# Optimization experiments

Measured on AMD Instinct MI355X. Metric: run time of the kernel, lower is better.

## Reference

```python
import jax, jax.numpy as jnp
import numpy as np

WH, WW = 8, 8
N_TOK = WH * WW
NUM_HEADS = 4
DIM = 128
B_WIN = 4096  # num_windows * B
NW = 64       # windows per image (for mask)


def _make_rel_tables():
    # relative coords table (1, 2*Wh-1, 2*Ww-1, 2), log-spaced as in SwinV2
    ch = np.arange(-(WH - 1), WH, dtype=np.float32)
    cw = np.arange(-(WW - 1), WW, dtype=np.float32)
    t = np.stack(np.meshgrid(ch, cw, indexing='ij'), axis=-1)[None]  # (1,15,15,2)
    t[..., 0] /= (WH - 1)
    t[..., 1] /= (WW - 1)
    t *= 8
    t = np.sign(t) * np.log2(np.abs(t) + 1.0) / np.log2(8)
    # relative position index (N, N)
    coords = np.stack(np.meshgrid(np.arange(WH), np.arange(WW), indexing='ij'))
    cf = coords.reshape(2, -1)
    rel = cf[:, :, None] - cf[:, None, :]
    rel = rel.transpose(1, 2, 0).copy()
    rel[:, :, 0] += WH - 1
    rel[:, :, 1] += WW - 1
    rel[:, :, 0] *= 2 * WW - 1
    idx = rel.sum(-1).astype(np.int32)
    return jnp.asarray(t), jnp.asarray(idx)


def setup_inputs() -> dict:
    key = jax.random.key(0)
    ks = jax.random.split(key, 8)
    table, idx = _make_rel_tables()
    return {
        'x': jax.random.normal(ks[0], (B_WIN, N_TOK, DIM), jnp.float32),
        'context': jax.random.normal(ks[1], (B_WIN, N_TOK, DIM), jnp.float32),
        'mask': jnp.zeros((NW, N_TOK, N_TOK), jnp.float32),
        'q_w': jax.random.normal(ks[2], (DIM, DIM), jnp.float32) * 0.02,
        'q_b': jnp.zeros((DIM,), jnp.float32),
        'kv_w': jax.random.normal(ks[3], (2 * DIM, DIM), jnp.float32) * 0.02,
        'v_b': jnp.zeros((DIM,), jnp.float32),
        'logit_scale': jnp.full((NUM_HEADS, 1, 1), np.log(10.0), jnp.float32),
        'cpb_w1': jax.random.normal(ks[4], (512, 2), jnp.float32) * 0.02,
        'cpb_b1': jnp.zeros((512,), jnp.float32),
        'cpb_w2': jax.random.normal(ks[5], (NUM_HEADS, 512), jnp.float32) * 0.02,
        'proj_w': jax.random.normal(ks[6], (DIM, DIM), jnp.float32) * 0.02,
        'proj_b': jnp.zeros((DIM,), jnp.float32),
        'rel_coords_table': table,
        'rel_pos_index': idx,
    }


def _l2norm(t, eps=1e-12):
    return t / jnp.maximum(jnp.linalg.norm(t, axis=-1, keepdims=True), eps)


def reference(x, context, mask, q_w, q_b, kv_w, v_b, logit_scale,
              cpb_w1, cpb_b1, cpb_w2, proj_w, proj_b,
              rel_coords_table, rel_pos_index):
    B_, N, C = x.shape
    H = NUM_HEADS
    hd = C // H
    # projections (kv bias = [zeros_like(v_b); v_b])
    q = x @ q_w.T + q_b
    kv_bias = jnp.concatenate([jnp.zeros_like(v_b), v_b])
    kv = context @ kv_w.T + kv_bias
    q = q.reshape(B_, N, H, hd).transpose(0, 2, 1, 3)          # (B_,H,N,hd)
    kv = kv.reshape(B_, N, 2, H, hd).transpose(2, 0, 3, 1, 4)  # (2,B_,H,N,hd)
    k, v = kv[0], kv[1]
    # cosine attention with clamped learned scale
    attn = jnp.einsum('bhnd,bhmd->bhnm', _l2norm(q), _l2norm(k))
    scale = jnp.exp(jnp.minimum(logit_scale, np.log(1.0 / 0.01)))  # (H,1,1)
    attn = attn * scale[None]
    # CPB-MLP relative position bias
    hidd = jax.nn.relu(rel_coords_table @ cpb_w1.T + cpb_b1)   # (1,15,15,512)
    table = (hidd @ cpb_w2.T).reshape(-1, H)                   # ((2Wh-1)(2Ww-1), H)
    bias = table[rel_pos_index.reshape(-1)].reshape(N, N, H)
    bias = 16.0 * jax.nn.sigmoid(bias.transpose(2, 0, 1))      # (H,N,N)
    attn = attn + bias[None]
    # shift mask
    nW = mask.shape[0]
    attn = attn.reshape(B_ // nW, nW, H, N, N) + mask[None, :, None]
    attn = attn.reshape(B_, H, N, N)
    attn = jax.nn.softmax(attn, axis=-1)
    out = jnp.einsum('bhnm,bhmd->bhnd', attn, v)
    out = out.transpose(0, 2, 1, 3).reshape(B_, N, C)
    return out @ proj_w.T + proj_b
```

## Files before the change

kernel.cpp:

```cpp
#include <hip/hip_runtime.h>
#include <hip/hip_bf16.h>

#define NT 64
#define DIM 128
#define NH 4
#define HD 32

typedef __attribute__((ext_vector_type(8))) short short8;
typedef __attribute__((ext_vector_type(4))) short short4v;
typedef __attribute__((ext_vector_type(8))) __bf16 bf16x8;
typedef __attribute__((ext_vector_type(4))) float floatx4;

__device__ __forceinline__ short f2bf(float f) {
  unsigned u = __builtin_bit_cast(unsigned, f);
  u += 0x7FFFu + ((u >> 16) & 1u);
  return (short)(u >> 16);
}

__device__ __forceinline__ bf16x8 ldsfrag(const short* p) {
  return __builtin_bit_cast(bf16x8, *(const short8*)p);
}

__device__ __forceinline__ bf16x8 wfrag(const float* p) {
  float4 a = *(const float4*)p;
  float4 b = *(const float4*)(p + 4);
  short8 v;
  v[0]=f2bf(a.x); v[1]=f2bf(a.y); v[2]=f2bf(a.z); v[3]=f2bf(a.w);
  v[4]=f2bf(b.x); v[5]=f2bf(b.y); v[6]=f2bf(b.z); v[7]=f2bf(b.w);
  return __builtin_bit_cast(bf16x8, v);
}

#define MFMA(a,b,c) __builtin_amdgcn_mfma_f32_16x16x32_bf16(a,b,c,0,0,0)

__device__ __forceinline__ void stage_tile(const float* __restrict__ src, short* dst_base, int tid) {
  int r = tid >> 2, c0 = (tid & 3) * 32;
  const float4* s = (const float4*)(src + r * DIM + c0);
  short* dst = dst_base + r * 136 + c0;
#pragma unroll
  for (int i = 0; i < 4; ++i) {
    float4 a = s[2*i], b = s[2*i+1];
    short8 v;
    v[0]=f2bf(a.x); v[1]=f2bf(a.y); v[2]=f2bf(a.z); v[3]=f2bf(a.w);
    v[4]=f2bf(b.x); v[5]=f2bf(b.y); v[6]=f2bf(b.z); v[7]=f2bf(b.w);
    *(short8*)(dst + i*8) = v;
  }
}

__global__ void cpb_bias_kernel(const float* __restrict__ table,
                                const float* __restrict__ w1,
                                const float* __restrict__ b1,
                                const float* __restrict__ w2,
                                const int*   __restrict__ idx,
                                float* __restrict__ bias_packed) {
  __shared__ float logits[225][4];
  int t = threadIdx.x;
  if (t < 225) {
    float t0 = table[2*t], t1 = table[2*t+1];
    float a0=0.f, a1=0.f, a2=0.f, a3=0.f;
    for (int j = 0; j < 512; ++j) {
      float h = fmaxf(0.f, t0 * w1[2*j] + t1 * w1[2*j+1] + b1[j]);
      a0 += h * w2[j];
      a1 += h * w2[512 + j];
      a2 += h * w2[1024 + j];
      a3 += h * w2[1536 + j];
    }
    logits[t][0]=a0; logits[t][1]=a1; logits[t][2]=a2; logits[t][3]=a3;
  }
  __syncthreads();
  for (int f = t; f < 16384; f += 256) {
    int i    = f & 3;
    int lane = (f >> 2) & 63;
    int nt   = (f >> 8) & 3;
    int mt   = (f >> 10) & 3;
    int h    = (f >> 12) & 3;
    int r = mt*16 + (lane >> 4)*4 + i;
    int c = nt*16 + (lane & 15);
    int p = idx[r*64 + c];
    float v = logits[p][h];
    bias_packed[f] = 16.f / (1.f + __expf(-v));
  }
}

__global__ __launch_bounds__(256, 2)
void swin_ctx_attn_kernel(const float* __restrict__ x, const float* __restrict__ ctx,
                          const float* __restrict__ mask,
                          const float* __restrict__ q_w, const float* __restrict__ q_b,
                          const float* __restrict__ kv_w, const float* __restrict__ v_b,
                          const float* __restrict__ logit_scale,
                          const float* __restrict__ proj_w, const float* __restrict__ proj_b,
                          const float* __restrict__ bias_p,
                          float* __restrict__ out) {
  __shared__ short lds[38400] __attribute__((aligned(16)));
  const int tid  = threadIdx.x;
  const int lane = tid & 63;
  const int w    = tid >> 6;
  const int b    = blockIdx.x;
  const int lr   = lane & 15;
  const int lg   = lane >> 4;

  short* stage = lds;
  short* hb    = lds + 8704 + w * 7424;
  short* qn    = hb;
  short* kn    = hb + 2560;
  short* attnb = hb;
  short* vT    = hb + 5120;

  stage_tile(x + (size_t)b * (NT*DIM), stage, tid);
  __syncthreads();

  {
    floatx4 acc[4][2] = {};
    for (int ks = 0; ks < 4; ++ks) {
      bf16x8 A[4];
#pragma unroll
      for (int mt = 0; mt < 4; ++mt)
        A[mt] = ldsfrag(stage + (mt*16 + lr)*136 + ks*32 + lg*8);
#pragma unroll
      for (int nt = 0; nt < 2; ++nt) {
        bf16x8 B = wfrag(q_w + (size_t)(w*32 + nt*16 + lr)*DIM + ks*32 + lg*8);
#pragma unroll
        for (int mt = 0; mt < 4; ++mt)
          acc[mt][nt] = MFMA(A[mt], B, acc[mt][nt]);
      }
    }
    float qb0 = q_b[w*32 + lr], qb1 = q_b[w*32 + 16 + lr];
#pragma unroll
    for (int mt = 0; mt < 4; ++mt) {
      floatx4 ss;
#pragma unroll
      for (int i = 0; i < 4; ++i) {
        acc[mt][0][i] += qb0; acc[mt][1][i] += qb1;
        ss[i] = acc[mt][0][i]*acc[mt][0][i] + acc[mt][1][i]*acc[mt][1][i];
      }
      for (int m = 1; m < 16; m <<= 1)
#pragma unroll
        for (int i = 0; i < 4; ++i) ss[i] += __shfl_xor(ss[i], m, 64);
#pragma unroll
      for (int i = 0; i < 4; ++i) {
        float sc = 1.0f / fmaxf(sqrtf(ss[i]), 1e-12f);
        int row = mt*16 + lg*4 + i;
        qn[row*40 + lr]      = f2bf(acc[mt][0][i] * sc);
        qn[row*40 + 16 + lr] = f2bf(acc[mt][1][i] * sc);
      }
    }
  }
  __syncthreads();

  stage_tile(ctx + (size_t)b * (NT*DIM), stage, tid);
  __syncthreads();

  {
    floatx4 acc[4][2] = {};
    for (int ks = 0; ks < 4; ++ks) {
      bf16x8 A[4];
#pragma unroll
      for (int mt = 0; mt < 4; ++mt)
        A[mt] = ldsfrag(stage + (mt*16 + lr)*136 + ks*32 + lg*8);
#pragma unroll
      for (int nt = 0; nt < 2; ++nt) {
        bf16x8 B = wfrag(kv_w + (size_t)(w*32 + nt*16 + lr)*DIM + ks*32 + lg*8);
#pragma unroll
        for (int mt = 0; mt < 4; ++mt)
          acc[mt][nt] = MFMA(A[mt], B, acc[mt][nt]);
      }
    }
#pragma unroll
    for (int mt = 0; mt < 4; ++mt) {
      floatx4 ss;
#pragma unroll
      for (int i = 0; i < 4; ++i)
        ss[i] = acc[mt][0][i]*acc[mt][0][i] + acc[mt][1][i]*acc[mt][1][i];
      for (int m = 1; m < 16; m <<= 1)
#pragma unroll
        for (int i = 0; i < 4; ++i) ss[i] += __shfl_xor(ss[i], m, 64);
#pragma unroll
      for (int i = 0; i < 4; ++i) {
        float sc = 1.0f / fmaxf(sqrtf(ss[i]), 1e-12f);
        int row = mt*16 + lg*4 + i;
        kn[row*40 + lr]      = f2bf(acc[mt][0][i] * sc);
        kn[row*40 + 16 + lr] = f2bf(acc[mt][1][i] * sc);
      }
    }
  }

  {
    floatx4 acc[4][2] = {};
    for (int ks = 0; ks < 4; ++ks) {
      bf16x8 A[4];
#pragma unroll
      for (int mt = 0; mt < 4; ++mt)
        A[mt] = ldsfrag(stage + (mt*16 + lr)*136 + ks*32 + lg*8);
#pragma unroll
      for (int nt = 0; nt < 2; ++nt) {
        bf16x8 B = wfrag(kv_w + (size_t)(DIM + w*32 + nt*16 + lr)*DIM + ks*32 + lg*8);
#pragma unroll
        for (int mt = 0; mt < 4; ++mt)
          acc[mt][nt] = MFMA(A[mt], B, acc[mt][nt]);
      }
    }
    float vb0 = v_b[w*32 + lr], vb1 = v_b[w*32 + 16 + lr];
#pragma unroll
    for (int mt = 0; mt < 4; ++mt)
#pragma unroll
      for (int nt = 0; nt < 2; ++nt) {
        float vb = nt ? vb1 : vb0;
        short4v s4;
#pragma unroll
        for (int i = 0; i < 4; ++i) s4[i] = f2bf(acc[mt][nt][i] + vb);
        *(short4v*)(vT + (nt*16 + lr)*72 + mt*16 + lg*4) = s4;
      }
  }
  asm volatile("s_waitcnt lgkmcnt(0)" ::: "memory");

  floatx4 sacc[4][4] = {};
  {
    bf16x8 A[4];
#pragma unroll
    for (int mt = 0; mt < 4; ++mt)
      A[mt] = ldsfrag(qn + (mt*16 + lr)*40 + lg*8);
#pragma unroll
    for (int nt = 0; nt < 4; ++nt) {
      bf16x8 B = ldsfrag(kn + (nt*16 + lr)*40 + lg*8);
#pragma unroll
      for (int mt = 0; mt < 4; ++mt)
        sacc[mt][nt] = MFMA(A[mt], B, sacc[mt][nt]);
    }
  }

  {
    float scl = expf(fminf(logit_scale[w], 4.605170185988091f));
    int wimg = b & 63;
#pragma unroll
    for (int mt = 0; mt < 4; ++mt)
#pragma unroll
      for (int nt = 0; nt < 4; ++nt) {
        floatx4 bias4 = ((const floatx4*)bias_p)[(w*16 + mt*4 + nt)*64 + lane];
#pragma unroll
        for (int i = 0; i < 4; ++i) {
          int r = mt*16 + lg*4 + i, c = nt*16 + lr;
          sacc[mt][nt][i] = sacc[mt][nt][i]*scl + bias4[i] + mask[((size_t)wimg*64 + r)*64 + c];
        }
      }
#pragma unroll
    for (int mt = 0; mt < 4; ++mt) {
      floatx4 rmax;
#pragma unroll
      for (int i = 0; i < 4; ++i)
        rmax[i] = fmaxf(fmaxf(sacc[mt][0][i], sacc[mt][1][i]), fmaxf(sacc[mt][2][i], sacc[mt][3][i]));
      for (int m = 1; m < 16; m <<= 1)
#pragma unroll
        for (int i = 0; i < 4; ++i) rmax[i] = fmaxf(rmax[i], __shfl_xor(rmax[i], m, 64));
      floatx4 rsum = {};
#pragma unroll
      for (int nt = 0; nt < 4; ++nt)
#pragma unroll
        for (int i = 0; i < 4; ++i) {
          sacc[mt][nt][i] = __expf(sacc[mt][nt][i] - rmax[i]);
          rsum[i] += sacc[mt][nt][i];
        }
      for (int m = 1; m < 16; m <<= 1)
#pragma unroll
        for (int i = 0; i < 4; ++i) rsum[i] += __shfl_xor(rsum[i], m, 64);
#pragma unroll
      for (int i = 0; i < 4; ++i) rsum[i] = 1.0f / rsum[i];
#pragma unroll
      for (int nt = 0; nt < 4; ++nt)
#pragma unroll
        for (int i = 0; i < 4; ++i) sacc[mt][nt][i] *= rsum[i];
    }
  }

#pragma unroll
  for (int mt = 0; mt < 4; ++mt)
#pragma unroll
    for (int nt = 0; nt < 4; ++nt)
#pragma unroll
      for (int i = 0; i < 4; ++i)
        attnb[(mt*16 + lg*4 + i)*72 + nt*16 + lr] = f2bf(sacc[mt][nt][i]);
  asm volatile("s_waitcnt lgkmcnt(0)" ::: "memory");

  floatx4 oacc[4][2] = {};
  for (int ks = 0; ks < 2; ++ks) {
    bf16x8 A[4];
#pragma unroll
    for (int mt = 0; mt < 4; ++mt)
      A[mt] = ldsfrag(attnb + (mt*16 + lr)*72 + ks*32 + lg*8);
#pragma unroll
    for (int nt = 0; nt < 2; ++nt) {
      bf16x8 B = ldsfrag(vT + (nt*16 + lr)*72 + ks*32 + lg*8);
#pragma unroll
      for (int mt = 0; mt < 4; ++mt)
        oacc[mt][nt] = MFMA(A[mt], B, oacc[mt][nt]);
    }
  }

  __syncthreads();
#pragma unroll
  for (int mt = 0; mt < 4; ++mt)
#pragma unroll
    for (int nt = 0; nt < 2; ++nt)
#pragma unroll
      for (int i = 0; i < 4; ++i)
        stage[(mt*16 + lg*4 + i)*136 + w*32 + nt*16 + lr] = f2bf(oacc[mt][nt][i]);
  __syncthreads();

  {
    floatx4 acc[4][2] = {};
    for (int ks = 0; ks < 4; ++ks) {
      bf16x8 A[4];
#pragma unroll
      for (int mt = 0; mt < 4; ++mt)
        A[mt] = ldsfrag(stage + (mt*16 + lr)*136 + ks*32 + lg*8);
#pragma unroll
      for (int nt = 0; nt < 2; ++nt) {
        bf16x8 B = wfrag(proj_w + (size_t)(w*32 + nt*16 + lr)*DIM + ks*32 + lg*8);
#pragma unroll
        for (int mt = 0; mt < 4; ++mt)
          acc[mt][nt] = MFMA(A[mt], B, acc[mt][nt]);
      }
    }
    float pb0 = proj_b[w*32 + lr], pb1 = proj_b[w*32 + 16 + lr];
    float* outp = out + (size_t)b * (NT*DIM);
#pragma unroll
    for (int mt = 0; mt < 4; ++mt)
#pragma unroll
      for (int nt = 0; nt < 2; ++nt) {
        float pb = nt ? pb1 : pb0;
#pragma unroll
        for (int i = 0; i < 4; ++i)
          outp[(mt*16 + lg*4 + i)*DIM + w*32 + nt*16 + lr] = acc[mt][nt][i] + pb;
      }
  }
}

extern "C" void kernel_launch(void* const* d_in, const int* in_sizes, int n_in,
                              void* d_out, int out_size, void* d_ws, size_t ws_size,
                              hipStream_t stream) {
  const float* x     = (const float*)d_in[0];
  const float* ctx   = (const float*)d_in[1];
  const float* mask  = (const float*)d_in[2];
  const float* q_w   = (const float*)d_in[3];
  const float* q_b   = (const float*)d_in[4];
  const float* kv_w  = (const float*)d_in[5];
  const float* v_b   = (const float*)d_in[6];
  const float* ls    = (const float*)d_in[7];
  const float* w1    = (const float*)d_in[8];
  const float* b1    = (const float*)d_in[9];
  const float* w2    = (const float*)d_in[10];
  const float* pw    = (const float*)d_in[11];
  const float* pb    = (const float*)d_in[12];
  const float* table = (const float*)d_in[13];
  const int*   idx   = (const int*)d_in[14];

  float* bias_p = (float*)d_ws;
  int B = in_sizes[0] / (NT * DIM);

  cpb_bias_kernel<<<1, 256, 0, stream>>>(table, w1, b1, w2, idx, bias_p);
  swin_ctx_attn_kernel<<<B, 256, 0, stream>>>(x, ctx, mask, q_w, q_b, kv_w, v_b,
                                              ls, pw, pb, bias_p, (float*)d_out);
}
```

Before: 321.8 us.

## Pre-convert weights to bf16 and split each head across two waves with 512 threads

```diff
diff --git a/kernel.cpp b/kernel.cpp
--- a/kernel.cpp
+++ b/kernel.cpp
@@ -21,314 +21,343 @@
   return __builtin_bit_cast(bf16x8, *(const short8*)p);
 }
 
-__device__ __forceinline__ bf16x8 wfrag(const float* p) {
-  float4 a = *(const float4*)p;
-  float4 b = *(const float4*)(p + 4);
-  short8 v;
-  v[0]=f2bf(a.x); v[1]=f2bf(a.y); v[2]=f2bf(a.z); v[3]=f2bf(a.w);
-  v[4]=f2bf(b.x); v[5]=f2bf(b.y); v[6]=f2bf(b.z); v[7]=f2bf(b.w);
-  return __builtin_bit_cast(bf16x8, v);
-}
-
 #define MFMA(a,b,c) __builtin_amdgcn_mfma_f32_16x16x32_bf16(a,b,c,0,0,0)
 
-__device__ __forceinline__ void stage_tile(const float* __restrict__ src, short* dst_base, int tid) {
-  int r = tid >> 2, c0 = (tid & 3) * 32;
-  const float4* s = (const float4*)(src + r * DIM + c0);
-  short* dst = dst_base + r * 136 + c0;
-#pragma unroll
-  for (int i = 0; i < 4; ++i) {
-    float4 a = s[2*i], b = s[2*i+1];
-    short8 v;
-    v[0]=f2bf(a.x); v[1]=f2bf(a.y); v[2]=f2bf(a.z); v[3]=f2bf(a.w);
-    v[4]=f2bf(b.x); v[5]=f2bf(b.y); v[6]=f2bf(b.z); v[7]=f2bf(b.w);
-    *(short8*)(dst + i*8) = v;
-  }
-}
-
-__global__ void cpb_bias_kernel(const float* __restrict__ table,
-                                const float* __restrict__ w1,
-                                const float* __restrict__ b1,
-                                const float* __restrict__ w2,
-                                const int*   __restrict__ idx,
-                                float* __restrict__ bias_packed) {
-  __shared__ float logits[225][4];
+__global__ void prep_kernel(const float* __restrict__ table,
+                            const float* __restrict__ w1,
+                            const float* __restrict__ b1,
+                            const float* __restrict__ w2,
+                            const int*   __restrict__ idx,
+                            const float* __restrict__ q_w,
+                            const float* __restrict__ kv_w,
+                            const float* __restrict__ proj_w,
+                            float* __restrict__ bias_packed,
+                            short* __restrict__ wbf) {
   int t = threadIdx.x;
-  if (t < 225) {
-    float t0 = table[2*t], t1 = table[2*t+1];
-    float a0=0.f, a1=0.f, a2=0.f, a3=0.f;
-    for (int j = 0; j < 512; ++j) {
-      float h = fmaxf(0.f, t0 * w1[2*j] + t1 * w1[2*j+1] + b1[j]);
-      a0 += h * w2[j];
-      a1 += h * w2[512 + j];
-      a2 += h * w2[1024 + j];
-      a3 += h * w2[1536 + j];
-    }
-    logits[t][0]=a0; logits[t][1]=a1; logits[t][2]=a2; logits[t][3]=a3;
-  }
-  __syncthreads();
-  for (int f = t; f < 16384; f += 256) {
-    int i    = f & 3;
-    int lane = (f >> 2) & 63;
-    int nt   = (f >> 8) & 3;
-    int mt   = (f >> 10) & 3;
-    int h    = (f >> 12) & 3;
-    int r = mt*16 + (lane >> 4)*4 + i;
-    int c = nt*16 + (lane & 15);
-    int p = idx[r*64 + c];
-    float v = logits[p][h];
-    bias_packed[f] = 16.f / (1.f + __expf(-v));
-  }
-}
-
-__global__ __launch_bounds__(256, 2)
+  if (blockIdx.x == 0) {
+    __shared__ float logits[225][4];
+    if (t < 225) {
+      float t0 = table[2*t], t1 = table[2*t+1];
+      float a0=0.f, a1=0.f, a2=0.f, a3=0.f;
+      for (int j = 0; j < 512; ++j) {
+        float h = fmaxf(0.f, t0 * w1[2*j] + t1 * w1[2*j+1] + b1[j]);
+        a0 += h * w2[j];
+        a1 += h * w2[512 + j];
+        a2 += h * w2[1024 + j];
+        a3 += h * w2[1536 + j];
+      }
+      logits[t][0]=a0; logits[t][1]=a1; logits[t][2]=a2; logits[t][3]=a3;
+    }
+    __syncthreads();
+    for (int f = t; f < 16384; f += 256) {
+      int i    = f & 3;
+      int lane = (f >> 2) & 63;
+      int nt   = (f >> 8) & 3;
+      int mt   = (f >> 10) & 3;
+      int h    = (f >> 12) & 3;
+      int r = mt*16 + (lane >> 4)*4 + i;
+      int c = nt*16 + (lane & 15);
+      int p = idx[r*64 + c];
+      float v = logits[p][h];
+      bias_packed[f] = 16.f / (1.f + __expf(-v));
+    }
+  } else {
+    int gidx = (blockIdx.x - 1) * 4096 + t * 16;
+    const float* src; int off;
+    if (gidx < 16384)      { src = q_w;    off = gidx; }
+    else if (gidx < 49152) { src = kv_w;   off = gidx - 16384; }
+    else                   { src = proj_w; off = gidx - 49152; }
+    const float4* s = (const float4*)(src + off);
+    short* dst = wbf + gidx;
+#pragma unroll
+    for (int i = 0; i < 2; ++i) {
+      float4 a = s[2*i], b = s[2*i+1];
+      short8 v;
+      v[0]=f2bf(a.x); v[1]=f2bf(a.y); v[2]=f2bf(a.z); v[3]=f2bf(a.w);
+      v[4]=f2bf(b.x); v[5]=f2bf(b.y); v[6]=f2bf(b.z); v[7]=f2bf(b.w);
+      *(short8*)(dst + i*8) = v;
+    }
+  }
+}
+
+__global__ __launch_bounds__(512, 4)
 void swin_ctx_attn_kernel(const float* __restrict__ x, const float* __restrict__ ctx,
                           const float* __restrict__ mask,
-                          const float* __restrict__ q_w, const float* __restrict__ q_b,
-                          const float* __restrict__ kv_w, const float* __restrict__ v_b,
+                          const short* __restrict__ wq, const float* __restrict__ q_b,
+                          const short* __restrict__ wkv, const float* __restrict__ v_b,
                           const float* __restrict__ logit_scale,
-                          const float* __restrict__ proj_w, const float* __restrict__ proj_b,
+                          const short* __restrict__ wproj, const float* __restrict__ proj_b,
                           const float* __restrict__ bias_p,
                           float* __restrict__ out) {
   __shared__ short lds[38400] __attribute__((aligned(16)));
   const int tid  = threadIdx.x;
   const int lane = tid & 63;
-  const int w    = tid >> 6;
+  const int wv   = tid >> 6;
+  const int h    = wv >> 1;
+  const int s    = wv & 1;
   const int b    = blockIdx.x;
   const int lr   = lane & 15;
   const int lg   = lane >> 4;
 
   short* stage = lds;
-  short* hb    = lds + 8704 + w * 7424;
+  short* hb    = lds + 8704 + h * 7424;
   short* qn    = hb;
   short* kn    = hb + 2560;
   short* attnb = hb;
   short* vT    = hb + 5120;
 
-  stage_tile(x + (size_t)b * (NT*DIM), stage, tid);
-  __syncthreads();
-
-  {
-    floatx4 acc[4][2] = {};
+  const int sr = tid >> 3, sc = (tid & 7) * 16;
+  {
+    const float4* sx = (const float4*)(x + (size_t)b * (NT*DIM) + sr*DIM + sc);
+    short* d = stage + sr*136 + sc;
+#pragma unroll
+    for (int i = 0; i < 2; ++i) {
+      float4 a = sx[2*i], bb = sx[2*i+1];
+      short8 v;
+      v[0]=f2bf(a.x); v[1]=f2bf(a.y); v[2]=f2bf(a.z); v[3]=f2bf(a.w);
+      v[4]=f2bf(bb.x); v[5]=f2bf(bb.y); v[6]=f2bf(bb.z); v[7]=f2bf(bb.w);
+      *(short8*)(d + i*8) = v;
+    }
+  }
+  float4 cr[4];
+  {
+    const float4* cs = (const float4*)(ctx + (size_t)b * (NT*DIM) + sr*DIM + sc);
+#pragma unroll
+    for (int i = 0; i < 4; ++i) cr[i] = cs[i];
+  }
+  __syncthreads();
+
+  {
+    floatx4 acc[2][2] = {};
     for (int ks = 0; ks < 4; ++ks) {
-      bf16x8 A[4];
-#pragma unroll
-      for (int mt = 0; mt < 4; ++mt)
-        A[mt] = ldsfrag(stage + (mt*16 + lr)*136 + ks*32 + lg*8);
-#pragma unroll
-      for (int nt = 0; nt < 2; ++nt) {
-        bf16x8 B = wfrag(q_w + (size_t)(w*32 + nt*16 + lr)*DIM + ks*32 + lg*8);
-#pragma unroll
-        for (int mt = 0; mt < 4; ++mt)
-          acc[mt][nt] = MFMA(A[mt], B, acc[mt][nt]);
-      }
-    }
-    float qb0 = q_b[w*32 + lr], qb1 = q_b[w*32 + 16 + lr];
-#pragma unroll
-    for (int mt = 0; mt < 4; ++mt) {
+      bf16x8 A[2];
+#pragma unroll
+      for (int m = 0; m < 2; ++m)
+        A[m] = ldsfrag(stage + (s*32 + m*16 + lr)*136 + ks*32 + lg*8);
+#pragma unroll
+      for (int nt = 0; nt < 2; ++nt) {
+        bf16x8 B = ldsfrag(wq + (h*32 + nt*16 + lr)*DIM + ks*32 + lg*8);
+#pragma unroll
+        for (int m = 0; m < 2; ++m)
+          acc[m][nt] = MFMA(A[m], B, acc[m][nt]);
+      }
+    }
+    float qb0 = q_b[h*32 + lr], qb1 = q_b[h*32 + 16 + lr];
+#pragma unroll
+    for (int m = 0; m < 2; ++m) {
       floatx4 ss;
 #pragma unroll
       for (int i = 0; i < 4; ++i) {
-        acc[mt][0][i] += qb0; acc[mt][1][i] += qb1;
-        ss[i] = acc[mt][0][i]*acc[mt][0][i] + acc[mt][1][i]*acc[mt][1][i];
-      }
-      for (int m = 1; m < 16; m <<= 1)
-#pragma unroll
-        for (int i = 0; i < 4; ++i) ss[i] += __shfl_xor(ss[i], m, 64);
+        acc[m][0][i] += qb0; acc[m][1][i] += qb1;
+        ss[i] = acc[m][0][i]*acc[m][0][i] + acc[m][1][i]*acc[m][1][i];
+      }
+      for (int mm = 1; mm < 16; mm <<= 1)
+#pragma unroll
+        for (int i = 0; i < 4; ++i) ss[i] += __shfl_xor(ss[i], mm, 64);
 #pragma unroll
       for (int i = 0; i < 4; ++i) {
-        float sc = 1.0f / fmaxf(sqrtf(ss[i]), 1e-12f);
-        int row = mt*16 + lg*4 + i;
-        qn[row*40 + lr]      = f2bf(acc[mt][0][i] * sc);
-        qn[row*40 + 16 + lr] = f2bf(acc[mt][1][i] * sc);
-      }
-    }
-  }
-  __syncthreads();
-
-  stage_tile(ctx + (size_t)b * (NT*DIM), stage, tid);
-  __syncthreads();
-
-  {
-    floatx4 acc[4][2] = {};
+        float sc2 = 1.0f / fmaxf(sqrtf(ss[i]), 1e-12f);
+        int row = s*32 + m*16 + lg*4 + i;
+        qn[row*40 + lr]      = f2bf(acc[m][0][i] * sc2);
+        qn[row*40 + 16 + lr] = f2bf(acc[m][1][i] * sc2);
+      }
+    }
+  }
+  __syncthreads();
+
+  {
+    short* d = stage + sr*136 + sc;
+#pragma unroll
+    for (int i = 0; i < 2; ++i) {
+      float4 a = cr[2*i], bb = cr[2*i+1];
+      short8 v;
+      v[0]=f2bf(a.x); v[1]=f2bf(a.y); v[2]=f2bf(a.z); v[3]=f2bf(a.w);
+      v[4]=f2bf(bb.x); v[5]=f2bf(bb.y); v[6]=f2bf(bb.z); v[7]=f2bf(bb.w);
+      *(short8*)(d + i*8) = v;
+    }
+  }
+  __syncthreads();
+
+  {
+    floatx4 acc[2][2] = {};
     for (int ks = 0; ks < 4; ++ks) {
-      bf16x8 A[4];
-#pragma unroll
-      for (int mt = 0; mt < 4; ++mt)
-        A[mt] = ldsfrag(stage + (mt*16 + lr)*136 + ks*32 + lg*8);
-#pragma unroll
-      for (int nt = 0; nt < 2; ++nt) {
-        bf16x8 B = wfrag(kv_w + (size_t)(w*32 + nt*16 + lr)*DIM + ks*32 + lg*8);
-#pragma unroll
-        for (int mt = 0; mt < 4; ++mt)
-          acc[mt][nt] = MFMA(A[mt], B, acc[mt][nt]);
-      }
-    }
-#pragma unroll
-    for (int mt = 0; mt < 4; ++mt) {
+      bf16x8 A[2];
+#pragma unroll
+      for (int m = 0; m < 2; ++m)
+        A[m] = ldsfrag(stage + (s*32 + m*16 + lr)*136 + ks*32 + lg*8);
+#pragma unroll
+      for (int nt = 0; nt < 2; ++nt) {
+        bf16x8 B = ldsfrag(wkv + (h*32 + nt*16 + lr)*DIM + ks*32 + lg*8);
+#pragma unroll
+        for (int m = 0; m < 2; ++m)
+          acc[m][nt] = MFMA(A[m], B, acc[m][nt]);
+      }
+    }
+#pragma unroll
+    for (int m = 0; m < 2; ++m) {
       floatx4 ss;
 #pragma unroll
       for (int i = 0; i < 4; ++i)
-        ss[i] = acc[mt][0][i]*acc[mt][0][i] + acc[mt][1][i]*acc[mt][1][i];
-      for (int m = 1; m < 16; m <<= 1)
-#pragma unroll
-        for (int i = 0; i < 4; ++i) ss[i] += __shfl_xor(ss[i], m, 64);
+        ss[i] = acc[m][0][i]*acc[m][0][i] + acc[m][1][i]*acc[m][1][i];
+      for (int mm = 1; mm < 16; mm <<= 1)
+#pragma unroll
+        for (int i = 0; i < 4; ++i) ss[i] += __shfl_xor(ss[i], mm, 64);
 #pragma unroll
       for (int i = 0; i < 4; ++i) {
-        float sc = 1.0f / fmaxf(sqrtf(ss[i]), 1e-12f);
-        int row = mt*16 + lg*4 + i;
-        kn[row*40 + lr]      = f2bf(acc[mt][0][i] * sc);
-        kn[row*40 + 16 + lr] = f2bf(acc[mt][1][i] * sc);
-      }
-    }
-  }
-
-  {
-    floatx4 acc[4][2] = {};
+        float sc2 = 1.0f / fmaxf(sqrtf(ss[i]), 1e-12f);
+        int row = s*32 + m*16 + lg*4 + i;
+        kn[row*40 + lr]      = f2bf(acc[m][0][i] * sc2);
+        kn[row*40 + 16 + lr] = f2bf(acc[m][1][i] * sc2);
+      }
+    }
+  }
+
+  {
+    floatx4 acc[2][2] = {};
     for (int ks = 0; ks < 4; ++ks) {
-      bf16x8 A[4];
-#pragma unroll
-      for (int mt = 0; mt < 4; ++mt)
-        A[mt] = ldsfrag(stage + (mt*16 + lr)*136 + ks*32 + lg*8);
-#pragma unroll
-      for (int nt = 0; nt < 2; ++nt) {
-        bf16x8 B = wfrag(kv_w + (size_t)(DIM + w*32 + nt*16 + lr)*DIM + ks*32 + lg*8);
-#pragma unroll
-        for (int mt = 0; mt < 4; ++mt)
-          acc[mt][nt] = MFMA(A[mt], B, acc[mt][nt]);
-      }
-    }
-    float vb0 = v_b[w*32 + lr], vb1 = v_b[w*32 + 16 + lr];
-#pragma unroll
-    for (int mt = 0; mt < 4; ++mt)
+      bf16x8 A[2];
+#pragma unroll
+      for (int m = 0; m < 2; ++m)
+        A[m] = ldsfrag(stage + (s*32 + m*16 + lr)*136 + ks*32 + lg*8);
+#pragma unroll
+      for (int nt = 0; nt < 2; ++nt) {
+        bf16x8 B = ldsfrag(wkv + (DIM + h*32 + nt*16 + lr)*DIM + ks*32 + lg*8);
+#pragma unroll
+        for (int m = 0; m < 2; ++m)
+          acc[m][nt] = MFMA(A[m], B, acc[m][nt]);
+      }
+    }
+    float vb0 = v_b[h*32 + lr], vb1 = v_b[h*32 + 16 + lr];
+#pragma unroll
+    for (int m = 0; m < 2; ++m)
 #pragma unroll
       for (int nt = 0; nt < 2; ++nt) {
         float vb = nt ? vb1 : vb0;
         short4v s4;
 #pragma unroll
-        for (int i = 0; i < 4; ++i) s4[i] = f2bf(acc[mt][nt][i] + vb);
-        *(short4v*)(vT + (nt*16 + lr)*72 + mt*16 + lg*4) = s4;
-      }
-  }
-  asm volatile("s_waitcnt lgkmcnt(0)" ::: "memory");
-
-  floatx4 sacc[4][4] = {};
-  {
-    bf16x8 A[4];
-#pragma unroll
-    for (int mt = 0; mt < 4; ++mt)
-      A[mt] = ldsfrag(qn + (mt*16 + lr)*40 + lg*8);
+        for (int i = 0; i < 4; ++i) s4[i] = f2bf(acc[m][nt][i] + vb);
+        *(short4v*)(vT + (nt*16 + lr)*72 + s*32 + m*16 + lg*4) = s4;
+      }
+  }
+  __syncthreads();
+
+  floatx4 sacc[2][4] = {};
+  {
+    bf16x8 A[2];
+#pragma unroll
+    for (int m = 0; m < 2; ++m)
+      A[m] = ldsfrag(qn + (s*32 + m*16 + lr)*40 + lg*8);
 #pragma unroll
     for (int nt = 0; nt < 4; ++nt) {
       bf16x8 B = ldsfrag(kn + (nt*16 + lr)*40 + lg*8);
 #pragma unroll
-      for (int mt = 0; mt < 4; ++mt)
-        sacc[mt][nt] = MFMA(A[mt], B, sacc[mt][nt]);
-    }
-  }
-
-  {
-    float scl = expf(fminf(logit_scale[w], 4.605170185988091f));
+      for (int m = 0; m < 2; ++m)
+        sacc[m][nt] = MFMA(A[m], B, sacc[m][nt]);
+    }
+  }
+  __syncthreads();
+
+  {
+    float scl = __expf(fminf(logit_scale[h], 4.605170185988091f));
     int wimg = b & 63;
 #pragma unroll
-    for (int mt = 0; mt < 4; ++mt)
+    for (int m = 0; m < 2; ++m)
 #pragma unroll
       for (int nt = 0; nt < 4; ++nt) {
-        floatx4 bias4 = ((const floatx4*)bias_p)[(w*16 + mt*4 + nt)*64 + lane];
+        floatx4 bias4 = ((const floatx4*)bias_p)[(h*16 + (s*2+m)*4 + nt)*64 + lane];
 #pragma unroll
         for (int i = 0; i < 4; ++i) {
-          int r = mt*16 + lg*4 + i, c = nt*16 + lr;
-          sacc[mt][nt][i] = sacc[mt][nt][i]*scl + bias4[i] + mask[((size_t)wimg*64 + r)*64 + c];
+          int r = s*32 + m*16 + lg*4 + i, c = nt*16 + lr;
+          sacc[m][nt][i] = sacc[m][nt][i]*scl + bias4[i] + mask[((size_t)wimg*64 + r)*64 + c];
         }
       }
 #pragma unroll
-    for (int mt = 0; mt < 4; ++mt) {
+    for (int m = 0; m < 2; ++m) {
       floatx4 rmax;
 #pragma unroll
       for (int i = 0; i < 4; ++i)
-        rmax[i] = fmaxf(fmaxf(sacc[mt][0][i], sacc[mt][1][i]), fmaxf(sacc[mt][2][i], sacc[mt][3][i]));
-      for (int m = 1; m < 16; m <<= 1)
-#pragma unroll
-        for (int i = 0; i < 4; ++i) rmax[i] = fmaxf(rmax[i], __shfl_xor(rmax[i], m, 64));
+        rmax[i] = fmaxf(fmaxf(sacc[m][0][i], sacc[m][1][i]), fmaxf(sacc[m][2][i], sacc[m][3][i]));
+      for (int mm = 1; mm < 16; mm <<= 1)
+#pragma unroll
+        for (int i = 0; i < 4; ++i) rmax[i] = fmaxf(rmax[i], __shfl_xor(rmax[i], mm, 64));
       floatx4 rsum = {};
 #pragma unroll
       for (int nt = 0; nt < 4; ++nt)
 #pragma unroll
         for (int i = 0; i < 4; ++i) {
-          sacc[mt][nt][i] = __expf(sacc[mt][nt][i] - rmax[i]);
-          rsum[i] += sacc[mt][nt][i];
+          sacc[m][nt][i] = __expf(sacc[m][nt][i] - rmax[i]);
+          rsum[i] += sacc[m][nt][i];
         }
-      for (int m = 1; m < 16; m <<= 1)
-#pragma unroll
-        for (int i = 0; i < 4; ++i) rsum[i] += __shfl_xor(rsum[i], m, 64);
+      for (int mm = 1; mm < 16; mm <<= 1)
+#pragma unroll
+        for (int i = 0; i < 4; ++i) rsum[i] += __shfl_xor(rsum[i], mm, 64);
 #pragma unroll
       for (int i = 0; i < 4; ++i) rsum[i] = 1.0f / rsum[i];
 #pragma unroll
       for (int nt = 0; nt < 4; ++nt)
 #pragma unroll
-        for (int i = 0; i < 4; ++i) sacc[mt][nt][i] *= rsum[i];
-    }
-  }
-
-#pragma unroll
-  for (int mt = 0; mt < 4; ++mt)
+        for (int i = 0; i < 4; ++i) sacc[m][nt][i] *= rsum[i];
+    }
+  }
+
+#pragma unroll
+  for (int m = 0; m < 2; ++m)
 #pragma unroll
     for (int nt = 0; nt < 4; ++nt)
 #pragma unroll
       for (int i = 0; i < 4; ++i)
-        attnb[(mt*16 + lg*4 + i)*72 + nt*16 + lr] = f2bf(sacc[mt][nt][i]);
+        attnb[(s*32 + m*16 + lg*4 + i)*72 + nt*16 + lr] = f2bf(sacc[m][nt][i]);
   asm volatile("s_waitcnt lgkmcnt(0)" ::: "memory");
 
-  floatx4 oacc[4][2] = {};
+  floatx4 oacc[2][2] = {};
   for (int ks = 0; ks < 2; ++ks) {
-    bf16x8 A[4];
-#pragma unroll
-    for (int mt = 0; mt < 4; ++mt)
-      A[mt] = ldsfrag(attnb + (mt*16 + lr)*72 + ks*32 + lg*8);
+    bf16x8 A[2];
+#pragma unroll
+    for (int m = 0; m < 2; ++m)
+      A[m] = ldsfrag(attnb + (s*32 + m*16 + lr)*72 + ks*32 + lg*8);
 #pragma unroll
     for (int nt = 0; nt < 2; ++nt) {
       bf16x8 B = ldsfrag(vT + (nt*16 + lr)*72 + ks*32 + lg*8);
 #pragma unroll
-      for (int mt = 0; mt < 4; ++mt)
-        oacc[mt][nt] = MFMA(A[mt], B, oacc[mt][nt]);
-    }
-  }
-
-  __syncthreads();
-#pragma unroll
-  for (int mt = 0; mt < 4; ++mt)
+      for (int m = 0; m < 2; ++m)
+        oacc[m][nt] = MFMA(A[m], B, oacc[m][nt]);
+    }
+  }
+
+#pragma unroll
+  for (int m = 0; m < 2; ++m)
 #pragma unroll
     for (int nt = 0; nt < 2; ++nt)
 #pragma unroll
       for (int i = 0; i < 4; ++i)
-        stage[(mt*16 + lg*4 + i)*136 + w*32 + nt*16 + lr] = f2bf(oacc[mt][nt][i]);
-  __syncthreads();
-
-  {
-    floatx4 acc[4][2] = {};
+        stage[(s*32 + m*16 + lg*4 + i)*136 + h*32 + nt*16 + lr] = f2bf(oacc[m][nt][i]);
+  __syncthreads();
+
+  {
+    floatx4 acc[2][2] = {};
     for (int ks = 0; ks < 4; ++ks) {
-      bf16x8 A[4];
-#pragma unroll
-      for (int mt = 0; mt < 4; ++mt)
-        A[mt] = ldsfrag(stage + (mt*16 + lr)*136 + ks*32 + lg*8);
-#pragma unroll
-      for (int nt = 0; nt < 2; ++nt) {
-        bf16x8 B = wfrag(proj_w + (size_t)(w*32 + nt*16 + lr)*DIM + ks*32 + lg*8);
-#pragma unroll
-        for (int mt = 0; mt < 4; ++mt)
-          acc[mt][nt] = MFMA(A[mt], B, acc[mt][nt]);
-      }
-    }
-    float pb0 = proj_b[w*32 + lr], pb1 = proj_b[w*32 + 16 + lr];
+      bf16x8 A[2];
+#pragma unroll
+      for (int m = 0; m < 2; ++m)
+        A[m] = ldsfrag(stage + (s*32 + m*16 + lr)*136 + ks*32 + lg*8);
+#pragma unroll
+      for (int nt = 0; nt < 2; ++nt) {
+        bf16x8 B = ldsfrag(wproj + (h*32 + nt*16 + lr)*DIM + ks*32 + lg*8);
+#pragma unroll
+        for (int m = 0; m < 2; ++m)
+          acc[m][nt] = MFMA(A[m], B, acc[m][nt]);
+      }
+    }
+    float pb0 = proj_b[h*32 + lr], pb1 = proj_b[h*32 + 16 + lr];
     float* outp = out + (size_t)b * (NT*DIM);
 #pragma unroll
-    for (int mt = 0; mt < 4; ++mt)
+    for (int m = 0; m < 2; ++m)
 #pragma unroll
       for (int nt = 0; nt < 2; ++nt) {
         float pb = nt ? pb1 : pb0;
 #pragma unroll
         for (int i = 0; i < 4; ++i)
-          outp[(mt*16 + lg*4 + i)*DIM + w*32 + nt*16 + lr] = acc[mt][nt][i] + pb;
+          outp[(s*32 + m*16 + lg*4 + i)*DIM + h*32 + nt*16 + lr] = acc[m][nt][i] + pb;
       }
   }
 }
@@ -353,9 +382,14 @@
   const int*   idx   = (const int*)d_in[14];
 
   float* bias_p = (float*)d_ws;
+  short* wbf    = (short*)((char*)d_ws + 65536);
+  short* wq     = wbf;
+  short* wkv    = wbf + 16384;
+  short* wproj  = wbf + 49152;
   int B = in_sizes[0] / (NT * DIM);
 
-  cpb_bias_kernel<<<1, 256, 0, stream>>>(table, w1, b1, w2, idx, bias_p);
-  swin_ctx_attn_kernel<<<B, 256, 0, stream>>>(x, ctx, mask, q_w, q_b, kv_w, v_b,
-                                              ls, pw, pb, bias_p, (float*)d_out);
-}
+  prep_kernel<<<17, 256, 0, stream>>>(table, w1, b1, w2, idx, q_w, kv_w, pw,
+                                      bias_p, wbf);
+  swin_ctx_attn_kernel<<<B, 512, 0, stream>>>(x, ctx, mask, wq, q_b, wkv, v_b,
+                                              ls, wproj, pb, bias_p, (float*)d_out);
+}
```

After: 273.1 us. -15.1%, faster.
